# Kernel optimization log

Hardware: AMD Instinct MI355X
Metric: run time of the kernel (lower is better)

The kernel has to match this reference:

```python
import jax, jax.numpy as jnp
import numpy as np

B = 8
C_IN = 3
IMG = 64
NF = 32
N_CALLS = 8
LAT = 512
KSIZES = [2 ** i + 1 for i in range(1, int(np.log2(IMG) - 1))]  # [3, 5, 9, 17]
N_SCALES = len(KSIZES)
C_FACTOR = 3 * N_SCALES          # identity + sobel-x + sobel-y per scale
GROUPS = C_FACTOR // 3           # 4
F = NF * C_FACTOR                # 384 expanded channels
CG = F // GROUPS                 # 96 channels per group
DK_TOT = 3 * GROUPS * CG * CG + 3 * F   # 111744 dynamic weights+biases
DK_HID = 2 * LAT                 # lat_factor = 2
OUT_CH = NF + NF + NF + 1        # 97 (multi_cut split sizes)
STATE = NF + NF * IMG + NF * IMG + IMG * IMG  # 8224


def _leaky(x):
    return jax.nn.leaky_relu(x, 0.2)


def _sobel_pair(k):
    c = jnp.linspace(-1.0, 1.0, k)
    gx = jnp.cos(0.5 * jnp.pi * c)[:, None] * jnp.sin(0.5 * jnp.pi * c)[None, :]
    return gx, gx.T


def sin_sobel(x):
    # fixed multi-scale depthwise sin-sobel filters, mode='split_out':
    # per scale concat [x, gx(x) all chans, gy(x) all chans]
    Bx, C, H, W = x.shape
    outs = []
    for k in KSIZES:
        gx, gy = _sobel_pair(k)
        w = jnp.broadcast_to(jnp.stack([gx, gy])[None], (C, 2, k, k)).reshape(C * 2, 1, k, k)
        p = (k - 1) // 2
        y = jax.lax.conv_general_dilated(x, w.astype(x.dtype), (1, 1), [(p, p), (p, p)],
                                         feature_group_count=C,
                                         dimension_numbers=('NCHW', 'OIHW', 'NCHW'))
        y = y.reshape(Bx, C, 2, H, W).transpose(0, 2, 1, 3, 4).reshape(Bx, 2 * C, H, W)
        outs.append(jnp.concatenate([x, y], axis=1))
    return jnp.concatenate(outs, axis=1)  # [B, 3*C*n_scales, H, W]


def instance_norm(x, eps=1e-5):
    m = x.mean(axis=(2, 3), keepdims=True)
    v = ((x - m) ** 2).mean(axis=(2, 3), keepdims=True)
    return (x - m) * jax.lax.rsqrt(v + eps)


def lin_res(x, Ws, bs, W0, b0, W1, b1):
    # LinearResidualBlock: shortcut + 0.1 * MLP
    return x @ Ws + bs + 0.1 * (_leaky(x @ W0 + b0) @ W1 + b1)


def conv1x1(x, w, b):
    return jnp.einsum('oi,bihw->bohw', w, x) + b[None, :, None, None]


def res_block(x, c0w, c0b, c1w, c1b, csw, csb):
    # ResidualBlock (1x1 convs): conv_s(x) + 0.1 * conv1(lrelu(conv0(lrelu(x))))
    dx = conv1x1(_leaky(x), c0w, c0b)
    dx = conv1x1(_leaky(dx), c1w, c1b)
    return conv1x1(x, csw, csb) + 0.1 * dx


def dyna_res_block(x, lat, Ws, bs, W0, b0, W1, b1):
    # DynaResidualBlock: per-sample grouped 1x1 conv weights generated from lat
    Bx, Fc, H, W = x.shape
    ks = lin_res(lat, Ws, bs, W0, b0, W1, b1)  # [B, DK_TOT]
    S = GROUPS * CG * CG
    k_in, k_mid, k_out, b_in, b_mid, b_out = jnp.split(
        ks, [S, 2 * S, 3 * S, 3 * S + Fc, 3 * S + 2 * Fc], axis=1)
    k_in = k_in.reshape(Bx, GROUPS, CG, CG)
    k_mid = k_mid.reshape(Bx, GROUPS, CG, CG)
    k_out = k_out.reshape(Bx, GROUPS, CG, CG)
    xg = x.reshape(Bx, GROUPS, CG, H, W)
    h = jnp.einsum('bgoi,bgihw->bgohw', k_in, xg) + b_in.reshape(Bx, GROUPS, CG, 1, 1)
    h = _leaky(h)
    h = jnp.einsum('bgoi,bgihw->bgohw', k_mid, h) + b_mid.reshape(Bx, GROUPS, CG, 1, 1)
    h = _leaky(h)
    h = jnp.einsum('bgoi,bgihw->bgohw', k_out, h) + b_out.reshape(Bx, GROUPS, CG, 1, 1)
    return x + h.reshape(Bx, Fc, H, W)  # identity shortcut (fin == fout)


def _forward(x, inj_lat, in_conv_w, in_conv_b, fl_Ws, fl_bs, fl_W0, fl_b0, fl_W1, fl_b1,
             dk_Ws, dk_bs, dk_W0, dk_b0, dk_W1, dk_b1,
             fc_c0w, fc_c0b, fc_c1w, fc_c1b, fc_csw, fc_csb,
             out_conv_w, out_conv_b, otl_w, otl_b):
    Bs = x.shape[0]
    out = conv1x1(x, in_conv_w, in_conv_b)
    out_embs = [out]
    lat = inj_lat
    for c in range(N_CALLS):
        lat = lat + 0.1 * lin_res(lat, fl_Ws[c], fl_bs[c], fl_W0[c], fl_b0[c], fl_W1[c], fl_b1[c])
        z = sin_sobel(out)
        z = instance_norm(z)
        z = z * jax.nn.sigmoid(dyna_res_block(z, lat, dk_Ws, dk_bs, dk_W0, dk_b0, dk_W1, dk_b1))
        z = res_block(z, fc_c0w, fc_c0b, fc_c1w, fc_c1b, fc_csw, fc_csb)
        out = out + 0.1 * z
        out_embs.append(out)
    # NOTE: source applies frac_conv(out) again here, but frac_conv expects
    # n_filter*c_factor (384) input channels while out has n_filter (32);
    # that line would raise in torch, so it is omitted (see notes).
    y = conv1x1(out, out_conv_w, out_conv_b)  # [B, 97, H, W]
    f, fh, fw, hw = jnp.split(y, [NF, 2 * NF, 3 * NF], axis=1)
    state = jnp.concatenate([
        f.mean(axis=(2, 3)),
        fh.mean(axis=3).reshape(Bs, -1),
        fw.mean(axis=2).reshape(Bs, -1),
        hw.reshape(Bs, -1),
    ], axis=1)  # [B, STATE]
    lat_out = state @ otl_w + otl_b
    return lat_out, jnp.stack(out_embs)


def setup_inputs():
    key = jax.random.key(0)
    ks = jax.random.split(key, 16)
    s = 0.02
    return {
        'x': jax.random.normal(ks[0], (B, C_IN, IMG, IMG), jnp.float32),
        'inj_lat': jax.random.normal(ks[1], (B, LAT), jnp.float32),
        'in_conv_w': jax.random.normal(ks[2], (NF, C_IN), jnp.float32) * s,
        'in_conv_b': jnp.zeros((NF,), jnp.float32),
        'fl_Ws': jax.random.normal(ks[3], (N_CALLS, LAT, LAT), jnp.float32) * s,
        'fl_bs': jnp.zeros((N_CALLS, LAT), jnp.float32),
        'fl_W0': jax.random.normal(ks[4], (N_CALLS, LAT, LAT), jnp.float32) * s,
        'fl_b0': jnp.zeros((N_CALLS, LAT), jnp.float32),
        'fl_W1': jax.random.normal(ks[5], (N_CALLS, LAT, LAT), jnp.float32) * s,
        'fl_b1': jnp.zeros((N_CALLS, LAT), jnp.float32),
        'dk_Ws': jax.random.normal(ks[6], (LAT, DK_TOT), jnp.float32) * s,
        'dk_bs': jnp.zeros((DK_TOT,), jnp.float32),
        'dk_W0': jax.random.normal(ks[7], (LAT, DK_HID), jnp.float32) * s,
        'dk_b0': jnp.zeros((DK_HID,), jnp.float32),
        'dk_W1': jax.random.normal(ks[8], (DK_HID, DK_TOT), jnp.float32) * s,
        'dk_b1': jnp.zeros((DK_TOT,), jnp.float32),
        'fc_c0w': jax.random.normal(ks[9], (F, F), jnp.float32) * s,
        'fc_c0b': jnp.zeros((F,), jnp.float32),
        'fc_c1w': jax.random.normal(ks[10], (NF, F), jnp.float32) * s,
        'fc_c1b': jnp.zeros((NF,), jnp.float32),
        'fc_csw': jax.random.normal(ks[11], (NF, F), jnp.float32) * s,
        'fc_csb': jnp.zeros((NF,), jnp.float32),
        'out_conv_w': jax.random.normal(ks[12], (OUT_CH, NF), jnp.float32) * s,
        'out_conv_b': jnp.zeros((OUT_CH,), jnp.float32),
        'otl_w': jax.random.normal(ks[13], (STATE, LAT), jnp.float32) * s,
        'otl_b': jnp.zeros((LAT,), jnp.float32),
    }


def reference(x, inj_lat, in_conv_w, in_conv_b, fl_Ws, fl_bs, fl_W0, fl_b0, fl_W1, fl_b1,
              dk_Ws, dk_bs, dk_W0, dk_b0, dk_W1, dk_b1,
              fc_c0w, fc_c0b, fc_c1w, fc_c1b, fc_csw, fc_csb,
              out_conv_w, out_conv_b, otl_w, otl_b):
    return _forward(x, inj_lat, in_conv_w, in_conv_b, fl_Ws, fl_bs, fl_W0, fl_b0, fl_W1, fl_b1,
                    dk_Ws, dk_bs, dk_W0, dk_b0, dk_W1, dk_b1,
                    fc_c0w, fc_c0b, fc_c1w, fc_c1b, fc_csw, fc_csb,
                    out_conv_w, out_conv_b, otl_w, otl_b)
```

## Files before the change

### kernel.cpp

```cpp
#include <hip/hip_runtime.h>

#define DEV __device__ __forceinline__

typedef __attribute__((ext_vector_type(4))) float  f32x4;
typedef __attribute__((ext_vector_type(8))) short  s16x8;
typedef __attribute__((ext_vector_type(4))) short  s16x4;

union FragU { s16x8 v; unsigned short h[8]; };
union U4    { s16x4 v; unsigned short h[4]; };

DEV float lrelu(float x){ return x > 0.f ? x : 0.2f*x; }
DEV unsigned short bfrne(float f){
    unsigned u = __builtin_bit_cast(unsigned, f);
    u += 0x7fffu + ((u>>16)&1u);
    return (unsigned short)(u>>16);
}
DEV float bf2f(unsigned short h){
    unsigned u = ((unsigned)h)<<16; return __builtin_bit_cast(float,u);
}
DEV f32x4 mfma16(s16x8 a, s16x8 b, f32x4 c){
    return __builtin_amdgcn_mfma_f32_16x16x32_bf16(a, b, c, 0, 0, 0);
}
DEV float wave_sum(float v){
    #pragma unroll
    for(int m=32;m>0;m>>=1) v += __shfl_xor(v, m, 64);
    return v;
}
DEV void blk_reduce2(float& a, float& b, float* sm){
    a = wave_sum(a); b = wave_sum(b);
    int wv = threadIdx.x>>6, ln = threadIdx.x&63;
    if(ln==0){ sm[wv*2]=a; sm[wv*2+1]=b; }
    __syncthreads();
    a = sm[0]+sm[2]+sm[4]+sm[6];
    b = sm[1]+sm[3]+sm[5]+sm[7];
    __syncthreads();
}

#define EMB   1048576
#define DKT   111744

__global__ __launch_bounds__(256) void k_init(
    float* state, float* latout, const float* otlb,
    float* lats, const float* inj,
    unsigned short* w016, const float* c0w,
    unsigned short* w116, const float* c1w,
    unsigned short* wcsh, unsigned short* wcsl, const float* csw)
{
    int i = blockIdx.x*256 + threadIdx.x;
    if(i < 65792){ state[i] = 0.f; return; }            i -= 65792;
    if(i < 4096){ latout[i] = otlb[i&511]; return; }    i -= 4096;
    if(i < 4096){ lats[i] = inj[i]; return; }           i -= 4096;
    if(i < 147456){
        int j = i&7, ln = (i>>3)&63, f2 = i>>9, mt = f2/12, kt = f2 - mt*12;
        w016[i] = bfrne(c0w[(mt*16 + (ln&15))*384 + kt*32 + (ln>>4)*8 + j]);
        return; }                                       i -= 147456;
    if(i < 12288){
        int j = i&7, ln = (i>>3)&63, f2 = i>>9, mt = f2/12, kt = f2 - mt*12;
        w116[i] = bfrne(c1w[(mt*16 + (ln&15))*384 + kt*32 + (ln>>4)*8 + j]);
        return; }                                       i -= 12288;
    if(i < 12288){
        int j = i&7, ln = (i>>3)&63, f2 = i>>9, mt = f2/12, kt = f2 - mt*12;
        wcsh[i] = bfrne(csw[(mt*16 + (ln&15))*384 + kt*32 + (ln>>4)*8 + j]);
        return; }                                       i -= 12288;
    if(i < 12288){
        int j = i&7, ln = (i>>3)&63, f2 = i>>9, mt = f2/12, kt = f2 - mt*12;
        float w = csw[(mt*16 + (ln&15))*384 + kt*32 + (ln>>4)*8 + j];
        unsigned short hh = bfrne(w);
        wcsl[i] = bfrne(w - bf2f(hh)); return; }
}

__global__ __launch_bounds__(256) void k_out0(const float* __restrict__ x,
    const float* __restrict__ w, const float* __restrict__ b, float* __restrict__ out0)
{
    int i = blockIdx.x*256 + threadIdx.x;
    int p = i & 4095, o = (i>>12)&31, bb = i>>17;
    const float* xb = x + (size_t)bb*12288 + p;
    out0[i] = b[o] + w[o*3]*xb[0] + w[o*3+1]*xb[4096] + w[o*3+2]*xb[8192];
}

__global__ __launch_bounds__(256) void k_latA(const float* __restrict__ lat,
    const float* __restrict__ Ws, const float* __restrict__ W0,
    float* __restrict__ ppS, float* __restrict__ ppH)
{
    __shared__ float ls[8][128];
    int t = threadIdx.x;
    int kb = blockIdx.y*128;
    for(int i=t;i<1024;i+=256) ls[i>>7][i&127] = lat[(i>>7)*512 + kb + (i&127)];
    __syncthreads();
    const float* W = blockIdx.z ? W0 : Ws;
    float* pp = blockIdx.z ? ppH : ppS;
    int j = blockIdx.x*128 + (t&127);
    int half = t>>7, klo = half*64;
    int p = blockIdx.y*2 + half;
    float acc[8] = {0,0,0,0,0,0,0,0};
    for(int kk=0;kk<64;kk++){
        float wv_ = W[(size_t)(kb+klo+kk)*512 + j];
        #pragma unroll
        for(int m=0;m<8;m++) acc[m] += ls[m][klo+kk]*wv_;
    }
    #pragma unroll
    for(int m=0;m<8;m++) pp[(size_t)(p*8+m)*512 + j] = acc[m];
}

__global__ __launch_bounds__(256) void k_latBC(const float* __restrict__ ppH,
    const float* __restrict__ flb0c,
    const float* __restrict__ W1, const float* __restrict__ b1c,
    const float* __restrict__ latc, const float* __restrict__ ppS,
    const float* __restrict__ flbsc, float* __restrict__ latn)
{
    __shared__ float lh[8][512];
    __shared__ float part[8][128];
    int t = threadIdx.x;
    for(int i=t;i<4096;i+=256){
        int m = i>>9, jj = i&511;
        float v = flb0c[jj];
        #pragma unroll
        for(int p=0;p<8;p++) v += ppH[(size_t)(p*8+m)*512 + jj];
        lh[m][jj] = lrelu(v);
    }
    __syncthreads();
    int j = blockIdx.x*128 + (t&127), half = t>>7;
    float acc[8] = {0,0,0,0,0,0,0,0};
    int k0 = half*256;
    for(int kk=k0;kk<k0+256;kk++){
        float w = W1[(size_t)kk*512 + j];
        #pragma unroll
        for(int m=0;m<8;m++) acc[m] += lh[m][kk]*w;
    }
    if(half==1){
        #pragma unroll
        for(int m=0;m<8;m++) part[m][t&127] = acc[m];
    }
    __syncthreads();
    if(half==0){
        #pragma unroll
        for(int m=0;m<8;m++){
            float sv = flbsc[j];
            #pragma unroll
            for(int p=0;p<8;p++) sv += ppS[(size_t)(p*8+m)*512 + j];
            float t1 = acc[m] + part[m][t&127] + b1c[j];
            latn[m*512+j] = latc[m*512+j] + 0.1f*sv + 0.01f*t1;
        }
    }
}

__global__ __launch_bounds__(256) void k_dkH(const float* __restrict__ latsAll,
    const float* __restrict__ W0, float* __restrict__ ppD)
{
    __shared__ float ls[64][128];
    int t = threadIdx.x;
    int kb = blockIdx.y*128;
    for(int i=t;i<8192;i+=256) ls[i>>7][i&127] = latsAll[(i>>7)*512 + kb + (i&127)];
    __syncthreads();
    int j = blockIdx.x*128 + (t&127);
    int ksub = t>>7;
    int p = blockIdx.y*2 + ksub;
    for(int mc=0;mc<4;mc++){
        float acc[16] = {0,0,0,0,0,0,0,0,0,0,0,0,0,0,0,0};
        for(int kk=0;kk<64;kk++){
            float wv_ = W0[(size_t)(kb + ksub*64 + kk)*1024 + j];
            #pragma unroll
            for(int mi=0;mi<16;mi++) acc[mi] += ls[mc*16+mi][ksub*64+kk]*wv_;
        }
        #pragma unroll
        for(int mi=0;mi<16;mi++) ppD[(size_t)(p*64 + mc*16+mi)*1024 + j] = acc[mi];
    }
}

__global__ __launch_bounds__(256) void k_dkAcvt(const float* __restrict__ latsAll,
    const float* __restrict__ ppD, const float* __restrict__ dkb0,
    unsigned short* __restrict__ Ahi, unsigned short* __restrict__ Alo)
{
    int i = blockIdx.x*256 + threadIdx.x;
    int m = i/1536, k = i - m*1536;
    float v;
    if(k < 512) v = latsAll[m*512 + k];
    else {
        int j = k - 512;
        float hv = dkb0[j];
        #pragma unroll
        for(int p=0;p<8;p++) hv += ppD[(size_t)(p*64+m)*1024 + j];
        v = 0.1f*lrelu(hv);
    }
    unsigned short hh = bfrne(v);
    Ahi[i] = hh; Alo[i] = bfrne(v - bf2f(hh));
}

__global__ __launch_bounds__(256) void k_dkMain(const unsigned short* __restrict__ Ahi,
    const unsigned short* __restrict__ Alo,
    const float* __restrict__ Wsb, const float* __restrict__ W1b,
    const float* __restrict__ bs, const float* __restrict__ b1,
    unsigned short* __restrict__ KSfh, unsigned short* __restrict__ KSfl,
    float* __restrict__ KSb32)
{
    __shared__ unsigned short Wh[64][138];
    __shared__ unsigned short Wl[64][138];
    __shared__ unsigned short Ah[64][72];
    __shared__ unsigned short Al[64][72];
    int t = threadIdx.x, wv = t>>6, lane = t&63, l15 = lane&15, lg = lane>>4, lkb = lg*8;
    int n0 = blockIdx.x*128;
    int sk = t>>5, sc = (t&31)*4;
    int am = t>>2, ac = (t&3)*16;

    f32x4 wreg[8];
    s16x8 ah0, ah1, al0, al1;
    {
        #pragma unroll
        for(int s=0;s<8;s++)
            wreg[s] = *(const f32x4*)(Wsb + (size_t)(sk + s*8)*DKT + n0 + sc);
        const unsigned short* Abh = Ahi + am*1536 + ac;
        const unsigned short* Abl = Alo + am*1536 + ac;
        ah0 = *(const s16x8*)(Abh);     ah1 = *(const s16x8*)(Abh + 8);
        al0 = *(const s16x8*)(Abl);     al1 = *(const s16x8*)(Abl + 8);
    }

    f32x4 acc[4][2];
    #pragma unroll
    for(int mt=0;mt<4;mt++){ acc[mt][0]=f32x4{0,0,0,0}; acc[mt][1]=f32x4{0,0,0,0}; }

    for(int kt=0;kt<24;kt++){
        #pragma unroll
        for(int s=0;s<8;s++){
            int k = sk + s*8;
            unsigned short hh[4], ll[4];
            #pragma unroll
            for(int e=0;e<4;e++){
                float w = wreg[s][e];
                hh[e] = bfrne(w); ll[e] = bfrne(w - bf2f(hh[e]));
            }
            *(unsigned*)(&Wh[k][sc])   = (unsigned)hh[0] | ((unsigned)hh[1]<<16);
            *(unsigned*)(&Wh[k][sc+2]) = (unsigned)hh[2] | ((unsigned)hh[3]<<16);
            *(unsigned*)(&Wl[k][sc])   = (unsigned)ll[0] | ((unsigned)ll[1]<<16);
            *(unsigned*)(&Wl[k][sc+2]) = (unsigned)ll[2] | ((unsigned)ll[3]<<16);
        }
        *(s16x8*)(&Ah[am][ac]) = ah0;  *(s16x8*)(&Ah[am][ac+8]) = ah1;
        *(s16x8*)(&Al[am][ac]) = al0;  *(s16x8*)(&Al[am][ac+8]) = al1;
        __syncthreads();
        if(kt < 23){
            int kn = kt+1;
            const float* Wb = (kn<8) ? (Wsb + (size_t)(kn*64)*DKT)
                                     : (W1b + (size_t)(kn*64-512)*DKT);
            #pragma unroll
            for(int s=0;s<8;s++)
                wreg[s] = *(const f32x4*)(Wb + (size_t)(sk + s*8)*DKT + n0 + sc);
            const unsigned short* Abh = Ahi + am*1536 + kn*64 + ac;
            const unsigned short* Abl = Alo + am*1536 + kn*64 + ac;
            ah0 = *(const s16x8*)(Abh);     ah1 = *(const s16x8*)(Abh + 8);
            al0 = *(const s16x8*)(Abl);     al1 = *(const s16x8*)(Abl + 8);
        }
        #pragma unroll
        for(int ks=0;ks<2;ks++){
            s16x8 afh[4], afl[4];
            #pragma unroll
            for(int mt=0;mt<4;mt++){
                afh[mt] = *(const s16x8*)(&Ah[mt*16+l15][ks*32+lkb]);
                afl[mt] = *(const s16x8*)(&Al[mt*16+l15][ks*32+lkb]);
            }
            #pragma unroll
            for(int nt=0;nt<2;nt++){
                int col = wv*32 + nt*16 + l15;
                FragU bh, bl;
                #pragma unroll
                for(int j=0;j<8;j++){
                    bh.h[j] = Wh[ks*32+lkb+j][col];
                    bl.h[j] = Wl[ks*32+lkb+j][col];
                }
                #pragma unroll
                for(int mt=0;mt<4;mt++){
                    acc[mt][nt] = mfma16(afh[mt], bh.v, acc[mt][nt]);
                    acc[mt][nt] = mfma16(afh[mt], bl.v, acc[mt][nt]);
                    acc[mt][nt] = mfma16(afl[mt], bh.v, acc[mt][nt]);
                }
            }
        }
        __syncthreads();
    }
    #pragma unroll
    for(int nt=0;nt<2;nt++){
        int n = n0 + wv*32 + nt*16 + l15;
        float bias = bs[n] + 0.1f*b1[n];
        bool isW = (n < 110592);
        size_t colpart = 0; int nb2 = 0;
        if(isW){
            int L = n / 36864, rem = n - L*36864;
            int g = rem / 9216; int rem2 = rem - g*9216;
            int oo = rem2 / 96; int kk = rem2 - oo*96;
            int lane2 = (((kk&31)>>3)<<4) + (oo&15);
            int f = (oo>>4)*3 + (kk>>5);
            colpart = ((((size_t)(g*3 + L))*18 + f)*64 + lane2)*8 + (kk&7);
        } else nb2 = n - 110592;
        #pragma unroll
        for(int mt=0;mt<4;mt++)
            #pragma unroll
            for(int q=0;q<4;q++){
                int row = mt*16 + lg*4 + q;
                float v = acc[mt][nt][q] + bias;
                unsigned short hh = bfrne(v);
                if(isW){
                    size_t dst = (size_t)row*110592 + colpart;
                    KSfh[dst] = hh;
                    KSfl[dst] = bfrne(v - bf2f(hh));
                } else {
                    KSb32[(size_t)row*1152 + nb2] = v;
                }
            }
    }
}

__global__ __launch_bounds__(256) void k_stat(const float* __restrict__ outPrev,
    float2* __restrict__ stats, float* __restrict__ gxy)
{
    __shared__ float img[4096], va[4096], vb[4096];
    __shared__ float ct[17], stp[17];
    __shared__ float red[8];
    int t = threadIdx.x, ch = blockIdx.x, b = blockIdx.y;
    const float* src = outPrev + ((size_t)b*32 + ch)*4096;
    float2* stc = stats + (b*32 + ch)*9;
    float* gb = gxy + ((size_t)(b*32 + ch)*8)*4096;
    for(int i=t;i<4096;i+=256) img[i] = src[i];
    __syncthreads();
    float s0=0.f, s1=0.f;
    for(int i=t;i<4096;i+=256){ float v=img[i]; s0+=v; s1+=v*v; }
    blk_reduce2(s0, s1, red);
    float mu = s0*(1.f/4096.f);
    float var = s1*(1.f/4096.f) - mu*mu; var = var<0.f?0.f:var;
    if(t==0) stc[0] = make_float2(mu, rsqrtf(var + 1e-5f));
    const int ksz[4] = {3,5,9,17};
    for(int s=0;s<4;s++){
        int k = ksz[s], p = (k-1)>>1;
        if(t < k){
            float cc = -1.f + 2.f*(float)t/(float)(k-1);
            ct[t]  = cosf(1.5707963267948966f*cc);
            stp[t] = sinf(1.5707963267948966f*cc);
        }
        __syncthreads();
        for(int i=t;i<4096;i+=256){
            int y = i>>6, x = i&63; float ac=0.f, as=0.f;
            for(int tt=0;tt<k;tt++){
                int yy = y+tt-p;
                if(yy>=0 && yy<64){ float f = img[yy*64+x]; ac += ct[tt]*f; as += stp[tt]*f; }
            }
            va[i]=ac; vb[i]=as;
        }
        __syncthreads();
        float gx0=0.f,gx1=0.f,gy0=0.f,gy1=0.f;
        float* g0 = gb + (size_t)(2*s)*4096;
        float* g1 = gb + (size_t)(2*s+1)*4096;
        for(int i=t;i<4096;i+=256){
            int y=i>>6, x=i&63; float gx=0.f, gy=0.f;
            for(int tt=0;tt<k;tt++){
                int xx = x+tt-p;
                if(xx>=0 && xx<64){ gx += stp[tt]*va[y*64+xx]; gy += ct[tt]*vb[y*64+xx]; }
            }
            g0[i] = gx; g1[i] = gy;
            gx0+=gx; gx1+=gx*gx; gy0+=gy; gy1+=gy*gy;
        }
        blk_reduce2(gx0, gx1, red);
        blk_reduce2(gy0, gy1, red);
        float mgx = gx0*(1.f/4096.f), vgx = gx1*(1.f/4096.f)-mgx*mgx; vgx=vgx<0.f?0.f:vgx;
        float mgy = gy0*(1.f/4096.f), vgy = gy1*(1.f/4096.f)-mgy*mgy; vgy=vgy<0.f?0.f:vgy;
        if(t==0){
            stc[1+2*s] = make_float2(mgx, rsqrtf(vgx+1e-5f));
            stc[2+2*s] = make_float2(mgy, rsqrtf(vgy+1e-5f));
        }
        __syncthreads();
    }
}

__global__ __launch_bounds__(512) void k_mega(const float* __restrict__ outPrev,
    const float2* __restrict__ stats, const float* __restrict__ gxy,
    const unsigned short* __restrict__ KSfh, const unsigned short* __restrict__ KSfl,
    const float* __restrict__ KSb32,
    const unsigned short* __restrict__ w016, const unsigned short* __restrict__ w116,
    const unsigned short* __restrict__ wcsh, const unsigned short* __restrict__ wcsl,
    const float* __restrict__ c0b, const float* __restrict__ c1b,
    const float* __restrict__ csb,
    float* __restrict__ outNext, int cCall)
{
    __shared__ __align__(16) unsigned short zth[12][64][32];
    __shared__ __align__(16) unsigned short ztl[12][64][32];
    __shared__ __align__(16) unsigned short lhf[25600];
    __shared__ float2 sst[288];
    int t = threadIdx.x, x = t&63, cq = t>>6;
    int y = blockIdx.x, b = blockIdx.y;
    const float* ob = outPrev + (size_t)b*131072;
    for(int i=t;i<288;i+=512) sst[i] = stats[b*288 + i];
    __syncthreads();
    #pragma unroll
    for(int i=0;i<4;i++){
        int ch = cq*4 + i;
        float v = ob[(size_t)ch*4096 + y*64 + x];
        float2 sr = sst[ch*9];
        float z = (v - sr.x)*sr.y;
        unsigned short hh = bfrne(z), hl = bfrne(z - bf2f(hh));
        #pragma unroll
        for(int s=0;s<4;s++){ zth[3*s][x][ch] = hh; ztl[3*s][x][ch] = hl; }
        const float* gsrc = gxy + ((size_t)(b*32 + ch)*8)*4096 + y*64 + x;
        #pragma unroll
        for(int s=0;s<4;s++){
            float gx = gsrc[(size_t)(2*s)*4096];
            float gy = gsrc[(size_t)(2*s+1)*4096];
            float2 sx = sst[ch*9 + 1+2*s], sy = sst[ch*9 + 2+2*s];
            float zx = (gx - sx.x)*sx.y, zy = (gy - sy.x)*sy.y;
            unsigned short hx = bfrne(zx), hy = bfrne(zy);
            zth[3*s+1][x][ch] = hx; ztl[3*s+1][x][ch] = bfrne(zx - bf2f(hx));
            zth[3*s+2][x][ch] = hy; ztl[3*s+2][x][ch] = bfrne(zy - bf2f(hy));
        }
    }
    __syncthreads();

    int lane = t&63, l15 = lane&15, lg = lane>>4, lkb = lg*8, w = cq;
    int pxslot = w&3, half = w>>2;
    int row = cCall*8 + b;
    int pxl = pxslot*16 + l15;
    unsigned short* lhh = &lhf[w*3200];
    unsigned short* lhl = &lhf[w*3200 + 1600];
    #pragma unroll 1
    for(int gi=0; gi<2; gi++){
        int g = half*2 + gi;
        const unsigned short* Kfh = KSfh + (size_t)((row*4 + g)*3)*9216;
        const unsigned short* Kfl = KSfl + (size_t)((row*4 + g)*3)*9216;
        const float* Bf = KSb32 + (size_t)row*1152 + g*96;

        f32x4 acc[6];
        #pragma unroll
        for(int mt=0;mt<6;mt++) acc[mt]=f32x4{0,0,0,0};
        #pragma unroll
        for(int kt=0;kt<3;kt++){
            s16x8 bh = *(const s16x8*)(&zth[g*3+kt][pxl][lkb]);
            s16x8 bl = *(const s16x8*)(&ztl[g*3+kt][pxl][lkb]);
            #pragma unroll
            for(int mt=0;mt<6;mt++){
                s16x8 ah = *(const s16x8*)(Kfh + ((mt*3+kt)*64 + lane)*8);
                s16x8 al = *(const s16x8*)(Kfl + ((mt*3+kt)*64 + lane)*8);
                acc[mt] = mfma16(ah, bh, acc[mt]);
                acc[mt] = mfma16(ah, bl, acc[mt]);
                acc[mt] = mfma16(al, bh, acc[mt]);
            }
        }
        #pragma unroll
        for(int mt=0;mt<6;mt++){
            int o0 = mt*16 + lg*4;
            f32x4 bb = *(const f32x4*)(Bf + o0);
            U4 hh, hl;
            #pragma unroll
            for(int q=0;q<4;q++){
                float v = lrelu(acc[mt][q] + bb[q]);
                hh.h[q] = bfrne(v); hl.h[q] = bfrne(v - bf2f(hh.h[q]));
            }
            *(s16x4*)(&lhh[l15*100 + o0]) = hh.v;
            *(s16x4*)(&lhl[l15*100 + o0]) = hl.v;
        }
        #pragma unroll
        for(int mt=0;mt<6;mt++) acc[mt]=f32x4{0,0,0,0};
        #pragma unroll
        for(int kt=0;kt<3;kt++){
            s16x8 bh = *(const s16x8*)(&lhh[l15*100 + kt*32+lkb]);
            s16x8 bl = *(const s16x8*)(&lhl[l15*100 + kt*32+lkb]);
            #pragma unroll
            for(int mt=0;mt<6;mt++){
                s16x8 ah = *(const s16x8*)(Kfh + 9216 + ((mt*3+kt)*64 + lane)*8);
                s16x8 al = *(const s16x8*)(Kfl + 9216 + ((mt*3+kt)*64 + lane)*8);
                acc[mt] = mfma16(ah, bh, acc[mt]);
                acc[mt] = mfma16(ah, bl, acc[mt]);
                acc[mt] = mfma16(al, bh, acc[mt]);
            }
        }
        #pragma unroll
        for(int mt=0;mt<6;mt++){
            int o0 = mt*16 + lg*4;
            f32x4 bb = *(const f32x4*)(Bf + 384 + o0);
            U4 hh, hl;
            #pragma unroll
            for(int q=0;q<4;q++){
                float v = lrelu(acc[mt][q] + bb[q]);
                hh.h[q] = bfrne(v); hl.h[q] = bfrne(v - bf2f(hh.h[q]));
            }
            *(s16x4*)(&lhh[l15*100 + o0]) = hh.v;
            *(s16x4*)(&lhl[l15*100 + o0]) = hl.v;
        }
        #pragma unroll
        for(int mt=0;mt<6;mt++) acc[mt]=f32x4{0,0,0,0};
        #pragma unroll
        for(int kt=0;kt<3;kt++){
            s16x8 bh = *(const s16x8*)(&lhh[l15*100 + kt*32+lkb]);
            s16x8 bl = *(const s16x8*)(&lhl[l15*100 + kt*32+lkb]);
            #pragma unroll
            for(int mt=0;mt<6;mt++){
                s16x8 ah = *(const s16x8*)(Kfh + 18432 + ((mt*3+kt)*64 + lane)*8);
                s16x8 al = *(const s16x8*)(Kfl + 18432 + ((mt*3+kt)*64 + lane)*8);
                acc[mt] = mfma16(ah, bh, acc[mt]);
                acc[mt] = mfma16(ah, bl, acc[mt]);
                acc[mt] = mfma16(al, bh, acc[mt]);
            }
        }
        #pragma unroll
        for(int mt=0;mt<6;mt++){
            int o0 = mt*16 + lg*4;
            f32x4 bb = *(const f32x4*)(Bf + 768 + o0);
            int part = g*3 + (o0>>5), cc = o0&31;
            U4 zvh, zvl;
            zvh.v = *(const s16x4*)(&zth[part][pxl][cc]);
            zvl.v = *(const s16x4*)(&ztl[part][pxl][cc]);
            U4 ozh;
            #pragma unroll
            for(int q=0;q<4;q++){
                float zf = bf2f(zvh.h[q]) + bf2f(zvl.h[q]);
                float d  = zf + acc[mt][q] + bb[q];
                float sg = 1.f/(1.f + __expf(-d));
                ozh.h[q] = bfrne(zf*sg);
            }
            *(s16x4*)(&zth[part][pxl][cc]) = ozh.v;
        }
    }
    __syncthreads();

    unsigned short* ldx = &lhf[pxslot*6272];
    f32x4 a1[12];
    #pragma unroll
    for(int lm=0;lm<12;lm++) a1[lm]=f32x4{0,0,0,0};
    #pragma unroll 1
    for(int kt=0;kt<12;kt++){
        FragU bzh, blz;
        bzh.v = *(const s16x8*)(&zth[kt][pxl][lkb]);
        #pragma unroll
        for(int j=0;j<8;j++) blz.h[j] = bfrne(lrelu(bf2f(bzh.h[j])));
        #pragma unroll
        for(int lm=0;lm<12;lm++){
            int mt = half*12 + lm;
            s16x8 af = *(const s16x8*)(w016 + ((size_t)(mt*12+kt)<<9) + (lane<<3));
            a1[lm] = mfma16(af, blz.v, a1[lm]);
        }
    }
    #pragma unroll
    for(int lm=0;lm<12;lm++){
        int mt = half*12 + lm;
        int o0 = mt*16 + lg*4;
        f32x4 bb = *(const f32x4*)(c0b + o0);
        U4 hv;
        #pragma unroll
        for(int q=0;q<4;q++) hv.h[q] = bfrne(lrelu(a1[lm][q] + bb[q]));
        *(s16x4*)(&ldx[l15*392 + o0]) = hv.v;
    }
    __syncthreads();

    {
        int mt = half;
        f32x4 a2 = f32x4{0,0,0,0};
        f32x4 a3 = f32x4{0,0,0,0};
        #pragma unroll 1
        for(int kt=0;kt<12;kt++){
            s16x8 bh_ = *(const s16x8*)(&ldx[l15*392 + kt*32 + lkb]);
            s16x8 bzh = *(const s16x8*)(&zth[kt][pxl][lkb]);
            s16x8 af1 = *(const s16x8*)(w116 + ((size_t)(mt*12+kt)<<9) + (lane<<3));
            a2 = mfma16(af1, bh_, a2);
            s16x8 wh = *(const s16x8*)(wcsh + ((size_t)(mt*12+kt)<<9) + (lane<<3));
            s16x8 wl = *(const s16x8*)(wcsl + ((size_t)(mt*12+kt)<<9) + (lane<<3));
            a3 = mfma16(wh, bzh, a3);
            a3 = mfma16(wl, bzh, a3);
        }
        int o0 = mt*16 + lg*4;
        #pragma unroll
        for(int q=0;q<4;q++){
            int o = o0+q;
            int px = y*64 + pxl;
            float dx2 = a2[q] + c1b[o];
            float r   = a3[q] + csb[o] + 0.1f*dx2;
            size_t oidx = (size_t)b*131072 + (size_t)o*4096 + px;
            outNext[oidx] = outPrev[oidx] + 0.1f*r;
        }
    }
}

__global__ __launch_bounds__(256) void k_head1(const float* __restrict__ outF,
    const float* __restrict__ wout, const float* __restrict__ bout, float* __restrict__ state)
{
    __shared__ float sw[97*32];
    __shared__ float sb_[97];
    __shared__ float fp[32];
    __shared__ float fwp[2048];
    int t = threadIdx.x, b = blockIdx.y, pxb = blockIdx.x*256;
    for(int i=t;i<97*32;i+=256) sw[i] = wout[i];
    if(t<97) sb_[t] = bout[t];
    if(t<32) fp[t] = 0.f;
    for(int i=t;i<2048;i+=256) fwp[i] = 0.f;
    __syncthreads();
    int px = pxb + t, lane = t&63, wv = t>>6;
    float xi[32];
    #pragma unroll
    for(int i=0;i<32;i++) xi[i] = outF[(size_t)b*131072 + (size_t)i*4096 + px];
    float* st = state + (size_t)b*8224;
    int row = (pxb>>6) + wv, x = lane;
    for(int o=0;o<97;o++){
        float acc = sb_[o];
        #pragma unroll
        for(int i=0;i<32;i++) acc += sw[o*32+i]*xi[i];
        if(o < 32){
            float s = wave_sum(acc);
            if(lane==0) atomicAdd(&fp[o], s);
        } else if(o < 64){
            float s = wave_sum(acc);
            if(lane==0) st[32 + (o-32)*64 + row] = s*(1.f/64.f);
        } else if(o < 96){
            atomicAdd(&fwp[(o-64)*64 + x], acc);
        } else {
            st[4128 + px] = acc;
        }
    }
    __syncthreads();
    if(t<32) atomicAdd(&st[t], fp[t]*(1.f/4096.f));
    for(int i=t;i<2048;i+=256) atomicAdd(&st[2080+i], fwp[i]*(1.f/64.f));
}

__global__ __launch_bounds__(256) void k_head2(const float* __restrict__ state,
    const float* __restrict__ otlw, float* __restrict__ latout)
{
    __shared__ float ss[8*514];
    int t = threadIdx.x, j = blockIdx.x*256 + t, s0 = blockIdx.y*514;
    for(int i=t;i<8*514;i+=256){ int bb=i/514, si=i-bb*514; ss[i] = state[(size_t)bb*8224 + s0 + si]; }
    __syncthreads();
    float acc[8] = {0,0,0,0,0,0,0,0};
    for(int si=0;si<514;si++){
        float wv_ = otlw[(size_t)(s0+si)*512 + j];
        #pragma unroll
        for(int b2=0;b2<8;b2++) acc[b2] += ss[b2*514+si]*wv_;
    }
    #pragma unroll
    for(int b2=0;b2<8;b2++) atomicAdd(latout + b2*512 + j, acc[b2]);
}

extern "C" void kernel_launch(void* const* d_in, const int* in_sizes, int n_in,
                              void* d_out, int out_size, void* d_ws, size_t ws_size,
                              hipStream_t stream)
{
    const float* x    = (const float*)d_in[0];
    const float* inj  = (const float*)d_in[1];
    const float* icw  = (const float*)d_in[2];
    const float* icb  = (const float*)d_in[3];
    const float* flWs = (const float*)d_in[4];
    const float* flbs = (const float*)d_in[5];
    const float* flW0 = (const float*)d_in[6];
    const float* flb0 = (const float*)d_in[7];
    const float* flW1 = (const float*)d_in[8];
    const float* flb1 = (const float*)d_in[9];
    const float* dkWs = (const float*)d_in[10];
    const float* dkbs = (const float*)d_in[11];
    const float* dkW0 = (const float*)d_in[12];
    const float* dkb0 = (const float*)d_in[13];
    const float* dkW1 = (const float*)d_in[14];
    const float* dkb1 = (const float*)d_in[15];
    const float* c0w  = (const float*)d_in[16];
    const float* c0b  = (const float*)d_in[17];
    const float* c1w  = (const float*)d_in[18];
    const float* c1b  = (const float*)d_in[19];
    const float* csw  = (const float*)d_in[20];
    const float* csb  = (const float*)d_in[21];
    const float* ocw  = (const float*)d_in[22];
    const float* ocb  = (const float*)d_in[23];
    const float* otlw = (const float*)d_in[24];
    const float* otlb = (const float*)d_in[25];
    float* out = (float*)d_out;

    char* wp = (char*)d_ws;
    auto carve = [&](size_t bytes)->void*{ void* p = wp; wp += (bytes + 255) & ~(size_t)255; return p; };
    float* lats  = (float*)carve(36864*4);
    float* ppS   = (float*)carve(32768*4);
    float* ppH   = (float*)carve(32768*4);
    float* ppD   = (float*)carve(524288*4);
    float* state = (float*)carve(65792*4);
    float2* stats = (float2*)carve(2304*8);
    float* gxy   = (float*)carve((size_t)8388608*4);
    unsigned short* Ahi   = (unsigned short*)carve((size_t)98304*2);
    unsigned short* Alo   = (unsigned short*)carve((size_t)98304*2);
    unsigned short* KSfh  = (unsigned short*)carve((size_t)7077888*2);
    unsigned short* KSfl  = (unsigned short*)carve((size_t)7077888*2);
    float*          KSb32 = (float*)carve((size_t)73728*4);
    unsigned short* w016  = (unsigned short*)carve((size_t)147456*2);
    unsigned short* w116  = (unsigned short*)carve((size_t)12288*2);
    unsigned short* wcsh  = (unsigned short*)carve((size_t)12288*2);
    unsigned short* wcsl  = (unsigned short*)carve((size_t)12288*2);

    k_init<<<1009,256,0,stream>>>(state, out, otlb, lats, inj,
                                  w016, c0w, w116, c1w, wcsh, wcsl, csw);
    k_out0<<<4096,256,0,stream>>>(x, icw, icb, out + 4096);

    for(int c=0;c<8;c++){
        const float* latc = lats + c*4096;
        k_latA<<<dim3(4,4,2),256,0,stream>>>(latc, flWs + (size_t)c*262144, flW0 + (size_t)c*262144,
                                             ppS, ppH);
        k_latBC<<<4,256,0,stream>>>(ppH, flb0 + (size_t)c*512,
                                    flW1 + (size_t)c*262144, flb1 + (size_t)c*512,
                                    latc, ppS, flbs + (size_t)c*512, lats + (c+1)*4096);
    }

    k_dkH<<<dim3(8,4),256,0,stream>>>(lats + 4096, dkW0, ppD);
    k_dkAcvt<<<384,256,0,stream>>>(lats + 4096, ppD, dkb0, Ahi, Alo);
    k_dkMain<<<873,256,0,stream>>>(Ahi, Alo, dkWs, dkW1, dkbs, dkb1, KSfh, KSfl, KSb32);

    for(int c=0;c<8;c++){
        const float* outPrev = out + 4096 + (size_t)c*EMB;
        float*       outNext = out + 4096 + (size_t)(c+1)*EMB;
        k_stat<<<dim3(32,8),256,0,stream>>>(outPrev, stats, gxy);
        k_mega<<<dim3(64,8),512,0,stream>>>(outPrev, stats, gxy, KSfh, KSfl, KSb32,
                                            w016, w116, wcsh, wcsl,
                                            c0b, c1b, csb, outNext, c);
    }

    k_head1<<<dim3(16,8),256,0,stream>>>(out + 4096 + (size_t)8*EMB, ocw, ocb, state);
    k_head2<<<dim3(2,16),256,0,stream>>>(state, otlw, out);
}
```

Baseline: 2.416 ms.

## Swizzle z-tile LDS layout, vectorize its stores, and reshape latent MLP kernels

Applies an XOR swizzle to the channel index of the zth/ztl LDS tiles and writes four channels per thread as a single 64-bit store. This is meant to cut LDS bank conflicts and the number of scalar LDS stores in k_mega. It also reshapes k_latA into 128-thread blocks with more blocks, and restructures k_latBC so each block handles one latent row across 512 threads, which raises parallelism in these small serial kernels. Loop unroll pragmas are added in the latent and dk kernels as well. The swizzle must be applied identically on every read and write path, or results will be wrong.

After: 2.532 ms. +4.8%, slower.

```diff
diff --git a/kernel.cpp b/kernel.cpp
--- a/kernel.cpp
+++ b/kernel.cpp
@@ -78,70 +78,55 @@
     out0[i] = b[o] + w[o*3]*xb[0] + w[o*3+1]*xb[4096] + w[o*3+2]*xb[8192];
 }
 
-__global__ __launch_bounds__(256) void k_latA(const float* __restrict__ lat,
+__global__ __launch_bounds__(128) void k_latA(const float* __restrict__ lat,
     const float* __restrict__ Ws, const float* __restrict__ W0,
     float* __restrict__ ppS, float* __restrict__ ppH)
 {
-    __shared__ float ls[8][128];
+    __shared__ float ls[8][64];
     int t = threadIdx.x;
-    int kb = blockIdx.y*128;
-    for(int i=t;i<1024;i+=256) ls[i>>7][i&127] = lat[(i>>7)*512 + kb + (i&127)];
+    int p = blockIdx.y;
+    int kb = (p>>1)*128, klo = (p&1)*64;
+    for(int i=t;i<512;i+=128) ls[i>>6][i&63] = lat[(i>>6)*512 + kb + klo + (i&63)];
     __syncthreads();
     const float* W = blockIdx.z ? W0 : Ws;
     float* pp = blockIdx.z ? ppH : ppS;
-    int j = blockIdx.x*128 + (t&127);
-    int half = t>>7, klo = half*64;
-    int p = blockIdx.y*2 + half;
+    int j = blockIdx.x*128 + t;
     float acc[8] = {0,0,0,0,0,0,0,0};
+    #pragma unroll 8
     for(int kk=0;kk<64;kk++){
         float wv_ = W[(size_t)(kb+klo+kk)*512 + j];
         #pragma unroll
-        for(int m=0;m<8;m++) acc[m] += ls[m][klo+kk]*wv_;
+        for(int m=0;m<8;m++) acc[m] += ls[m][kk]*wv_;
     }
     #pragma unroll
     for(int m=0;m<8;m++) pp[(size_t)(p*8+m)*512 + j] = acc[m];
 }
 
-__global__ __launch_bounds__(256) void k_latBC(const float* __restrict__ ppH,
+__global__ __launch_bounds__(512) void k_latBC(const float* __restrict__ ppH,
     const float* __restrict__ flb0c,
     const float* __restrict__ W1, const float* __restrict__ b1c,
     const float* __restrict__ latc, const float* __restrict__ ppS,
     const float* __restrict__ flbsc, float* __restrict__ latn)
 {
-    __shared__ float lh[8][512];
-    __shared__ float part[8][128];
-    int t = threadIdx.x;
-    for(int i=t;i<4096;i+=256){
-        int m = i>>9, jj = i&511;
-        float v = flb0c[jj];
-        #pragma unroll
-        for(int p=0;p<8;p++) v += ppH[(size_t)(p*8+m)*512 + jj];
-        lh[m][jj] = lrelu(v);
-    }
-    __syncthreads();
-    int j = blockIdx.x*128 + (t&127), half = t>>7;
-    float acc[8] = {0,0,0,0,0,0,0,0};
-    int k0 = half*256;
-    for(int kk=k0;kk<k0+256;kk++){
-        float w = W1[(size_t)kk*512 + j];
-        #pragma unroll
-        for(int m=0;m<8;m++) acc[m] += lh[m][kk]*w;
-    }
-    if(half==1){
-        #pragma unroll
-        for(int m=0;m<8;m++) part[m][t&127] = acc[m];
-    }
-    __syncthreads();
-    if(half==0){
-        #pragma unroll
-        for(int m=0;m<8;m++){
-            float sv = flbsc[j];
-            #pragma unroll
-            for(int p=0;p<8;p++) sv += ppS[(size_t)(p*8+m)*512 + j];
-            float t1 = acc[m] + part[m][t&127] + b1c[j];
-            latn[m*512+j] = latc[m*512+j] + 0.1f*sv + 0.01f*t1;
-        }
-    }
+    __shared__ float lh[512];
+    int t = threadIdx.x, m = blockIdx.x, j = t;
+    {
+        float v = flb0c[t];
+        #pragma unroll
+        for(int p=0;p<8;p++) v += ppH[(size_t)(p*8+m)*512 + t];
+        lh[t] = lrelu(v);
+    }
+    __syncthreads();
+    float acc0 = 0.f, acc1 = 0.f;
+    #pragma unroll 8
+    for(int kk=0;kk<256;kk++)   acc0 += lh[kk]*W1[(size_t)kk*512 + j];
+    #pragma unroll 8
+    for(int kk=256;kk<512;kk++) acc1 += lh[kk]*W1[(size_t)kk*512 + j];
+    float sv = flbsc[j];
+    #pragma unroll
+    for(int p=0;p<8;p++) sv += ppS[(size_t)(p*8+m)*512 + j];
+    float t1 = acc0 + acc1 + b1c[j];
+    latn[m*512+j] = latc[m*512+j] + 0.1f*sv + 0.01f*t1;
 }
 
 __global__ __launch_bounds__(256) void k_dkH(const float* __restrict__ latsAll,
@@ -157,6 +142,7 @@
     int p = blockIdx.y*2 + ksub;
     for(int mc=0;mc<4;mc++){
         float acc[16] = {0,0,0,0,0,0,0,0,0,0,0,0,0,0,0,0};
+        #pragma unroll 4
         for(int kk=0;kk<64;kk++){
             float wv_ = W0[(size_t)(kb + ksub*64 + kk)*1024 + j];
             #pragma unroll
@@ -367,6 +353,8 @@
     }
 }
 
+DEV int zswz(int px, int ch){ return ((((ch>>3) ^ px) & 3) << 3) | (ch & 7); }
+
 __global__ __launch_bounds__(512) void k_mega(const float* __restrict__ outPrev,
     const float2* __restrict__ stats, const float* __restrict__ gxy,
     const unsigned short* __restrict__ KSfh, const unsigned short* __restrict__ KSfl,
@@ -386,26 +374,41 @@
     const float* ob = outPrev + (size_t)b*131072;
     for(int i=t;i<288;i+=512) sst[i] = stats[b*288 + i];
     __syncthreads();
-    #pragma unroll
-    for(int i=0;i<4;i++){
-        int ch = cq*4 + i;
-        float v = ob[(size_t)ch*4096 + y*64 + x];
-        float2 sr = sst[ch*9];
-        float z = (v - sr.x)*sr.y;
-        unsigned short hh = bfrne(z), hl = bfrne(z - bf2f(hh));
-        #pragma unroll
-        for(int s=0;s<4;s++){ zth[3*s][x][ch] = hh; ztl[3*s][x][ch] = hl; }
-        const float* gsrc = gxy + ((size_t)(b*32 + ch)*8)*4096 + y*64 + x;
+    int qw = zswz(x, cq*4);
+    {
+        U4 idh, idl;
+        #pragma unroll
+        for(int i=0;i<4;i++){
+            int ch = cq*4 + i;
+            float v = ob[(size_t)ch*4096 + y*64 + x];
+            float2 sr = sst[ch*9];
+            float z = (v - sr.x)*sr.y;
+            idh.h[i] = bfrne(z); idl.h[i] = bfrne(z - bf2f(idh.h[i]));
+        }
         #pragma unroll
         for(int s=0;s<4;s++){
+            *(s16x4*)(&zth[3*s][x][qw]) = idh.v;
+            *(s16x4*)(&ztl[3*s][x][qw]) = idl.v;
+        }
+    }
+    #pragma unroll 1
+    for(int s=0;s<4;s++){
+        U4 xh, xl, yh, yl;
+        #pragma unroll
+        for(int i=0;i<4;i++){
+            int ch = cq*4 + i;
+            const float* gsrc = gxy + ((size_t)(b*32 + ch)*8)*4096 + y*64 + x;
             float gx = gsrc[(size_t)(2*s)*4096];
             float gy = gsrc[(size_t)(2*s+1)*4096];
             float2 sx = sst[ch*9 + 1+2*s], sy = sst[ch*9 + 2+2*s];
             float zx = (gx - sx.x)*sx.y, zy = (gy - sy.x)*sy.y;
-            unsigned short hx = bfrne(zx), hy = bfrne(zy);
-            zth[3*s+1][x][ch] = hx; ztl[3*s+1][x][ch] = bfrne(zx - bf2f(hx));
-            zth[3*s+2][x][ch] = hy; ztl[3*s+2][x][ch] = bfrne(zy - bf2f(hy));
-        }
+            xh.h[i] = bfrne(zx); xl.h[i] = bfrne(zx - bf2f(xh.h[i]));
+            yh.h[i] = bfrne(zy); yl.h[i] = bfrne(zy - bf2f(yh.h[i]));
+        }
+        *(s16x4*)(&zth[3*s+1][x][qw]) = xh.v;
+        *(s16x4*)(&ztl[3*s+1][x][qw]) = xl.v;
+        *(s16x4*)(&zth[3*s+2][x][qw]) = yh.v;
+        *(s16x4*)(&ztl[3*s+2][x][qw]) = yl.v;
     }
     __syncthreads();
 
@@ -413,6 +416,7 @@
     int pxslot = w&3, half = w>>2;
     int row = cCall*8 + b;
     int pxl = pxslot*16 + l15;
+    int zq = zswz(pxl, lkb);
     unsigned short* lhh = &lhf[w*3200];
     unsigned short* lhl = &lhf[w*3200 + 1600];
     #pragma unroll 1
@@ -427,8 +431,8 @@
         for(int mt=0;mt<6;mt++) acc[mt]=f32x4{0,0,0,0};
         #pragma unroll
         for(int kt=0;kt<3;kt++){
-            s16x8 bh = *(const s16x8*)(&zth[g*3+kt][pxl][lkb]);
-            s16x8 bl = *(const s16x8*)(&ztl[g*3+kt][pxl][lkb]);
+            s16x8 bh = *(const s16x8*)(&zth[g*3+kt][pxl][zq]);
+            s16x8 bl = *(const s16x8*)(&ztl[g*3+kt][pxl][zq]);
             #pragma unroll
             for(int mt=0;mt<6;mt++){
                 s16x8 ah = *(const s16x8*)(Kfh + ((mt*3+kt)*64 + lane)*8);
@@ -499,9 +503,10 @@
             int o0 = mt*16 + lg*4;
             f32x4 bb = *(const f32x4*)(Bf + 768 + o0);
             int part = g*3 + (o0>>5), cc = o0&31;
+            int zo = zswz(pxl, cc);
             U4 zvh, zvl;
-            zvh.v = *(const s16x4*)(&zth[part][pxl][cc]);
-            zvl.v = *(const s16x4*)(&ztl[part][pxl][cc]);
+            zvh.v = *(const s16x4*)(&zth[part][pxl][zo]);
+            zvl.v = *(const s16x4*)(&ztl[part][pxl][zo]);
             U4 ozh;
             #pragma unroll
             for(int q=0;q<4;q++){
@@ -510,7 +515,7 @@
                 float sg = 1.f/(1.f + __expf(-d));
                 ozh.h[q] = bfrne(zf*sg);
             }
-            *(s16x4*)(&zth[part][pxl][cc]) = ozh.v;
+            *(s16x4*)(&zth[part][pxl][zo]) = ozh.v;
         }
     }
     __syncthreads();
@@ -522,7 +527,7 @@
     #pragma unroll 1
     for(int kt=0;kt<12;kt++){
         FragU bzh, blz;
-        bzh.v = *(const s16x8*)(&zth[kt][pxl][lkb]);
+        bzh.v = *(const s16x8*)(&zth[kt][pxl][zq]);
         #pragma unroll
         for(int j=0;j<8;j++) blz.h[j] = bfrne(lrelu(bf2f(bzh.h[j])));
         #pragma unroll
@@ -551,7 +556,7 @@
         #pragma unroll 1
         for(int kt=0;kt<12;kt++){
             s16x8 bh_ = *(const s16x8*)(&ldx[l15*392 + kt*32 + lkb]);
-            s16x8 bzh = *(const s16x8*)(&zth[kt][pxl][lkb]);
+            s16x8 bzh = *(const s16x8*)(&zth[kt][pxl][zq]);
             s16x8 af1 = *(const s16x8*)(w116 + ((size_t)(mt*12+kt)<<9) + (lane<<3));
             a2 = mfma16(af1, bh_, a2);
             s16x8 wh = *(const s16x8*)(wcsh + ((size_t)(mt*12+kt)<<9) + (lane<<3));
@@ -686,9 +691,9 @@
 
     for(int c=0;c<8;c++){
         const float* latc = lats + c*4096;
-        k_latA<<<dim3(4,4,2),256,0,stream>>>(latc, flWs + (size_t)c*262144, flW0 + (size_t)c*262144,
+        k_latA<<<dim3(4,8,2),128,0,stream>>>(latc, flWs + (size_t)c*262144, flW0 + (size_t)c*262144,
                                              ppS, ppH);
-        k_latBC<<<4,256,0,stream>>>(ppH, flb0 + (size_t)c*512,
+        k_latBC<<<8,512,0,stream>>>(ppH, flb0 + (size_t)c*512,
                                     flW1 + (size_t)c*262144, flb1 + (size_t)c*512,
                                     latc, ppS, flbs + (size_t)c*512, lats + (c+1)*4096);
     }
```
